# Performance work log

Hardware: AMD Instinct MI355X
Metric: run time of the kernel (lower is better)

The kernel has to match this reference:

```python
import jax, jax.numpy as jnp
import numpy as np

N = 10000
E = 640000


def setup_inputs() -> dict:
    key = jax.random.key(0)
    k = jax.random.split(key, 6)
    x = jax.random.normal(k[0], (N, 128), dtype=jnp.float32)
    edge_index = jax.random.randint(k[1], (2, E), 0, N, dtype=jnp.int64)
    # Linear weights stored as [in, out] (torch stores [out, in]; math is x @ W.T + b)
    w1 = jax.random.normal(k[2], (128, 128), dtype=jnp.float32) * 0.05
    b1 = jax.random.normal(k[3], (128,), dtype=jnp.float32) * 0.05
    w2 = jax.random.normal(k[4], (128, 128), dtype=jnp.float32) * 0.05
    b2 = jax.random.normal(k[5], (128,), dtype=jnp.float32) * 0.05
    return {"x": x, "edge_index": edge_index, "w1": w1, "b1": b1, "w2": w2, "b2": b2}


def gin_conv(x, src, dst, w, b, eps=0.0):
    # aggregate: out[i] = sum over edges (src->dst=i) of x[src]
    agg = jax.ops.segment_sum(x[src], dst, num_segments=N)  # [N, d]
    h = (1.0 + eps) * x + agg
    return h @ w + b


def reference(x, edge_index, w1, b1, w2, b2):
    src, dst = edge_index[0], edge_index[1]
    h = gin_conv(x, src, dst, w1, b1)
    h = jax.nn.relu(h)
    h = gin_conv(h, src, dst, w2, b2)
    return jax.nn.log_softmax(h, axis=1)
```

## Files before the change

### kernel.cpp

```cpp
#include <hip/hip_runtime.h>
#include <cstdint>

#define NNODES 10000
#define FDIM 128
#define MAXDEG 192
#define NPB 157
#define NBIN 64
#define BINCAP 16384

typedef _Float16 h2v  __attribute__((ext_vector_type(2)));
typedef _Float16 f16x8 __attribute__((ext_vector_type(8)));
typedef float    f32x4 __attribute__((ext_vector_type(4)));

__device__ __align__(16)  int            g_binoff[NBIN];
__device__ __align__(16)  unsigned       g_binbuf[NBIN * BINCAP];
__device__ __align__(16)  int            g_cnt[NNODES];
__device__ __align__(16)  unsigned short g_bkt[NNODES * MAXDEG];
__device__ __align__(256) unsigned g_xh [(NNODES + 1) * FDIM / 2];
__device__ __align__(256) unsigned g_h1h[(NNODES + 1) * FDIM / 2];
__device__ __align__(16)  unsigned g_wf[2 * 8192];

__device__ inline h2v as_h2(unsigned u) { return __builtin_bit_cast(h2v, u); }
__device__ inline unsigned as_u(h2v v) { return __builtin_bit_cast(unsigned, v); }
__device__ inline unsigned pack_f16x2(float a, float b) {
  h2v v; v[0] = (_Float16)a; v[1] = (_Float16)b;
  return as_u(v);
}
__device__ inline void vadd4(uint4& a, const uint4& b) {
  a.x = as_u(as_h2(a.x) + as_h2(b.x));
  a.y = as_u(as_h2(a.y) + as_h2(b.y));
  a.z = as_u(as_h2(a.z) + as_h2(b.z));
  a.w = as_u(as_h2(a.w) + as_h2(b.w));
}

__global__ __launch_bounds__(512) void prep1_kernel(
    const float* __restrict__ x, const int* __restrict__ ei,
    const float* __restrict__ w1, const float* __restrict__ w2,
    int E_, int PBLK) {
  const int bid = blockIdx.x, tid = threadIdx.x;
  if (bid < PBLK) {
    __shared__ int lcnt[NBIN], lbase[NBIN];
    if (tid < NBIN) lcnt[tid] = 0;
    __syncthreads();
    int dv[8], sv[8], rk[8], bn[8];
#pragma unroll
    for (int k = 0; k < 8; ++k) {
      int e = bid * 4096 + k * 512 + tid;
      dv[k] = (e < E_) ? ei[E_ + e] : -1;
      sv[k] = (e < E_) ? ei[e] : 0;
    }
#pragma unroll
    for (int k = 0; k < 8; ++k) {
      if (dv[k] >= 0) {
        bn[k] = (unsigned)dv[k] / NPB;
        rk[k] = atomicAdd(&lcnt[bn[k]], 1);
      }
    }
    __syncthreads();
    if (tid < NBIN && lcnt[tid] > 0)
      lbase[tid] = atomicAdd(&g_binoff[tid], lcnt[tid]);
    __syncthreads();
#pragma unroll
    for (int k = 0; k < 8; ++k) {
      if (dv[k] >= 0) {
        int pos = lbase[bn[k]] + rk[k];
        if (pos < BINCAP)
          g_binbuf[bn[k] * BINCAP + pos] =
              ((unsigned)(dv[k] - bn[k] * NPB) << 16) | (unsigned)sv[k];
      }
    }
  } else if (bid < PBLK + 625) {
    int i = (bid - PBLK) * 512 + tid;
    if (i < NNODES * 32) {
      float4 v = *(const float4*)(x + 4 * (size_t)i);
      uint2 o; o.x = pack_f16x2(v.x, v.y); o.y = pack_f16x2(v.z, v.w);
      *(uint2*)(g_xh + 2 * (size_t)i) = o;
    }
  } else {
    int idx = (bid - PBLK - 625) * 512 + tid;
    if (idx < 4096) {
      const float* w = (idx >= 2048) ? w2 : w1;
      int s = idx & 2047;
      int sl = s & 63, nk = s >> 6;
      int n = nk >> 2, kc = nk & 3;
      int kbase = kc * 32 + (sl >> 4) * 8;
      int f = n * 16 + (sl & 15);
      unsigned d0 = pack_f16x2(w[(size_t)(kbase + 0) * FDIM + f],
                               w[(size_t)(kbase + 1) * FDIM + f]);
      unsigned d1 = pack_f16x2(w[(size_t)(kbase + 2) * FDIM + f],
                               w[(size_t)(kbase + 3) * FDIM + f]);
      unsigned d2 = pack_f16x2(w[(size_t)(kbase + 4) * FDIM + f],
                               w[(size_t)(kbase + 5) * FDIM + f]);
      unsigned d3 = pack_f16x2(w[(size_t)(kbase + 6) * FDIM + f],
                               w[(size_t)(kbase + 7) * FDIM + f]);
      *(uint4*)(g_wf + (idx >> 11) * 8192 + 4 * s) = make_uint4(d0, d1, d2, d3);
    }
  }
}

__global__ __launch_bounds__(512) void prep2_kernel() {
  __shared__ int lcnt[NPB];
  __shared__ __align__(16) unsigned short lbkt[NPB * MAXDEG];

  const int bid = blockIdx.x, tid = threadIdx.x;
  const int lo = bid * NPB;
  const int nn = (NNODES - lo < NPB) ? (NNODES - lo) : NPB;
  for (int i = tid; i < NPB; i += 512) lcnt[i] = 0;
  __syncthreads();

  int cnt = g_binoff[bid];
  if (cnt > BINCAP) cnt = BINCAP;
  const unsigned* buf = g_binbuf + (size_t)bid * BINCAP;
  for (int i = tid; i < cnt; i += 512) {
    unsigned p = buf[i];
    int rel = (int)(p >> 16);
    if (rel < nn) {
      int q = atomicAdd(&lcnt[rel], 1);
      if (q < MAXDEG) lbkt[rel * MAXDEG + q] = (unsigned short)(p & 0xffffu);
    }
  }
  __syncthreads();

  for (int i = tid; i < nn; i += 512)
    g_cnt[lo + i] = (lcnt[i] > MAXDEG) ? MAXDEG : lcnt[i];
  const int nq = nn * (MAXDEG / 8);
  const uint4* srcq = (const uint4*)lbkt;
  uint4* dstq = (uint4*)(g_bkt + (size_t)lo * MAXDEG);
  for (int i = tid; i < nq; i += 512) dstq[i] = srcq[i];
  if (tid == 0) g_binoff[bid] = 0;
}

template <int MODE>
__global__ __launch_bounds__(512) void gin_layer_kernel(
    const float* __restrict__ bvec,
    float* __restrict__ out_g) {
  const unsigned* __restrict__ xh = (MODE == 0) ? g_xh : g_h1h;

  __shared__ __align__(16) unsigned al[16 * 68];
  __shared__ __align__(16) unsigned cfu[8 * 132];

  const int tid = threadIdx.x;
  const int wave = tid >> 6, lane = tid & 63;
  const int quad = lane >> 4, m16 = lane & 15;
  const int node0 = blockIdx.x * 8;
  const int myn = node0 + wave;

  uint4 bf[4];
  {
    const unsigned* wfp = g_wf + (MODE ? 8192 : 0);
#pragma unroll
    for (int kc = 0; kc < 4; ++kc)
      bf[kc] = *(const uint4*)(wfp + ((wave * 4 + kc) * 64 + lane) * 4);
  }
  const float bb = bvec[wave * 16 + m16];

  for (int i2 = tid; i2 < 8 * 68; i2 += 512) al[8 * 68 + i2] = 0;

  uint4 self4 = *(const uint4*)(xh + (size_t)myn * 64 + (m16 << 2));
  const int deg = g_cnt[myn];

  const unsigned short* nb16 = g_bkt + (size_t)myn * MAXDEG;
  int idxr[3];
#pragma unroll
  for (int r = 0; r < 3; ++r) {
    int g = r * 64 + lane;
    idxr[r] = (g < deg) ? (int)nb16[g] : NNODES;
  }

  h2v a0 = as_h2(0u), a1 = as_h2(0u), a2 = as_h2(0u), a3 = as_h2(0u);
  const int nbat = (deg + 31) >> 5;
  for (int bt = 0; bt < nbat; ++bt) {
    const int r = bt >> 1;
    const int src = (r == 0) ? idxr[0] : ((r == 1) ? idxr[1] : idxr[2]);
    const int base = (bt & 1) << 5;
    uint4 t[8];
#pragma unroll
    for (int k = 0; k < 8; ++k) {
      int e = __builtin_amdgcn_ds_bpermute((base + 4 * k + quad) << 2, src);
      t[k] = *(const uint4*)(xh + (unsigned)((e << 6) | (m16 << 2)));
    }
#pragma unroll
    for (int st2 = 1; st2 < 8; st2 <<= 1)
#pragma unroll
      for (int k = 0; k < 8; k += 2 * st2) vadd4(t[k], t[k + st2]);
    a0 += as_h2(t[0].x); a1 += as_h2(t[0].y);
    a2 += as_h2(t[0].z); a3 += as_h2(t[0].w);
  }

  int rr;
  rr = __shfl_xor((int)as_u(a0), 16, 64); a0 += as_h2((unsigned)rr);
  rr = __shfl_xor((int)as_u(a0), 32, 64); a0 += as_h2((unsigned)rr);
  rr = __shfl_xor((int)as_u(a1), 16, 64); a1 += as_h2((unsigned)rr);
  rr = __shfl_xor((int)as_u(a1), 32, 64); a1 += as_h2((unsigned)rr);
  rr = __shfl_xor((int)as_u(a2), 16, 64); a2 += as_h2((unsigned)rr);
  rr = __shfl_xor((int)as_u(a2), 32, 64); a2 += as_h2((unsigned)rr);
  rr = __shfl_xor((int)as_u(a3), 16, 64); a3 += as_h2((unsigned)rr);
  rr = __shfl_xor((int)as_u(a3), 32, 64); a3 += as_h2((unsigned)rr);
  a0 += as_h2(self4.x); a1 += as_h2(self4.y);
  a2 += as_h2(self4.z); a3 += as_h2(self4.w);
  if (quad == 0)
    *(uint4*)(al + wave * 68 + (m16 << 2)) =
        make_uint4(as_u(a0), as_u(a1), as_u(a2), as_u(a3));
  __syncthreads();

  uint4 af[4];
#pragma unroll
  for (int kc = 0; kc < 4; ++kc)
    af[kc] = *(const uint4*)(al + m16 * 68 + kc * 16 + quad * 4);

  const int n = wave;
  f32x4 acc = {0.f, 0.f, 0.f, 0.f};
#pragma unroll
  for (int kc = 0; kc < 4; ++kc)
    acc = __builtin_amdgcn_mfma_f32_16x16x32_f16(
            __builtin_bit_cast(f16x8, af[kc]),
            __builtin_bit_cast(f16x8, bf[kc]), acc, 0, 0, 0);

  if (MODE == 0) {
    _Float16* ch = (_Float16*)cfu;
    const int f = n * 16 + m16;
    if (quad < 2) {
#pragma unroll
      for (int reg = 0; reg < 4; ++reg)
        ch[(quad * 4 + reg) * 136 + f] = (_Float16)fmaxf(acc[reg] + bb, 0.f);
    }
    __syncthreads();
    if (tid < 256) {
      const int row = tid >> 5, c2 = (tid & 31) * 2;
      uint2 v = *(const uint2*)(cfu + row * 68 + c2);
      *(uint2*)(&g_h1h[(size_t)(node0 + row) * 64 + c2]) = v;
    }
  } else {
    float* cf = (float*)cfu;
    const int f = n * 16 + m16;
    if (quad < 2) {
#pragma unroll
      for (int reg = 0; reg < 4; ++reg)
        cf[(quad * 4 + reg) * 132 + f] = acc[reg] + bb;
    }
    __syncthreads();
    if (tid < 256) {
      const int row = tid >> 5, li = tid & 31;
      const float* base = cf + row * 132 + li * 4;
      float4 a4 = *(const float4*)(base);
      float mx = fmaxf(fmaxf(a4.x, a4.y), fmaxf(a4.z, a4.w));
#pragma unroll
      for (int off = 16; off >= 1; off >>= 1)
        mx = fmaxf(mx, __shfl_xor(mx, off, 64));
      float s = (__expf(a4.x - mx) + __expf(a4.y - mx))
              + (__expf(a4.z - mx) + __expf(a4.w - mx));
#pragma unroll
      for (int off = 16; off >= 1; off >>= 1)
        s += __shfl_xor(s, off, 64);
      const float ls = mx + __logf(s);
      float* orow = out_g + (size_t)(node0 + row) * FDIM + li * 4;
      *(float4*)(orow) = make_float4(a4.x - ls, a4.y - ls, a4.z - ls, a4.w - ls);
    }
  }
}

extern "C" void kernel_launch(void* const* d_in, const int* in_sizes, int n_in,
                              void* d_out, int out_size, void* d_ws, size_t ws_size,
                              hipStream_t stream) {
  const float* x  = (const float*)d_in[0];
  const int*   ei = (const int*)d_in[1];
  const float* w1 = (const float*)d_in[2];
  const float* b1 = (const float*)d_in[3];
  const float* w2 = (const float*)d_in[4];
  const float* b2 = (const float*)d_in[5];
  float* out = (float*)d_out;

  const int E_ = in_sizes[1] / 2;
  const int PBLK = (E_ + 4095) / 4096;

  prep1_kernel<<<PBLK + 625 + 8, 512, 0, stream>>>(x, ei, w1, w2, E_, PBLK);
  prep2_kernel<<<NBIN, 512, 0, stream>>>();

  gin_layer_kernel<0><<<1250, 512, 0, stream>>>(b1, nullptr);
  gin_layer_kernel<1><<<1250, 512, 0, stream>>>(b2, out);
}
```

Baseline: 108.1 us.

## Double bucket bins, move conversions to bucket pass, pre-fill sentinel neighbors

Halves nodes per bin (128 bins) so the bucket-fill stage runs on more blocks with less work each. The x and weight fp16 conversions move from the edge-binning kernel into the bucket kernel, letting the binning kernel run only edge blocks. Neighbor lists are pre-filled with a sentinel node index in shared memory, so the layer kernel loads indices without a per-lane degree check and issues those loads earlier. This adds a shared-memory fill per bin, and the smaller BINCAP raises the chance of overflow on skewed graphs.

```diff
diff --git a/kernel.cpp b/kernel.cpp
--- a/kernel.cpp
+++ b/kernel.cpp
@@ -4,9 +4,10 @@
 #define NNODES 10000
 #define FDIM 128
 #define MAXDEG 192
-#define NPB 157
-#define NBIN 64
-#define BINCAP 16384
+#define NPB 79
+#define NBIN 128
+#define BINCAP 6144
+#define SENT16 0x27102710u
 
 typedef _Float16 h2v  __attribute__((ext_vector_type(2)));
 typedef _Float16 f16x8 __attribute__((ext_vector_type(8)));
@@ -34,50 +35,87 @@
 }
 
 __global__ __launch_bounds__(512) void prep1_kernel(
-    const float* __restrict__ x, const int* __restrict__ ei,
-    const float* __restrict__ w1, const float* __restrict__ w2,
-    int E_, int PBLK) {
+    const int* __restrict__ ei, int E_) {
+  __shared__ int lcnt[NBIN], lbase[NBIN];
   const int bid = blockIdx.x, tid = threadIdx.x;
-  if (bid < PBLK) {
-    __shared__ int lcnt[NBIN], lbase[NBIN];
-    if (tid < NBIN) lcnt[tid] = 0;
-    __syncthreads();
-    int dv[8], sv[8], rk[8], bn[8];
-#pragma unroll
-    for (int k = 0; k < 8; ++k) {
-      int e = bid * 4096 + k * 512 + tid;
-      dv[k] = (e < E_) ? ei[E_ + e] : -1;
-      sv[k] = (e < E_) ? ei[e] : 0;
-    }
-#pragma unroll
-    for (int k = 0; k < 8; ++k) {
-      if (dv[k] >= 0) {
-        bn[k] = (unsigned)dv[k] / NPB;
-        rk[k] = atomicAdd(&lcnt[bn[k]], 1);
+  if (tid < NBIN) lcnt[tid] = 0;
+  __syncthreads();
+  int dv[8], sv[8], rk[8], bn[8];
+#pragma unroll
+  for (int k = 0; k < 8; ++k) {
+    int e = bid * 4096 + k * 512 + tid;
+    dv[k] = (e < E_) ? ei[E_ + e] : -1;
+    sv[k] = (e < E_) ? ei[e] : 0;
+  }
+#pragma unroll
+  for (int k = 0; k < 8; ++k) {
+    if (dv[k] >= 0) {
+      bn[k] = (unsigned)dv[k] / NPB;
+      rk[k] = atomicAdd(&lcnt[bn[k]], 1);
+    }
+  }
+  __syncthreads();
+  if (tid < NBIN && lcnt[tid] > 0)
+    lbase[tid] = atomicAdd(&g_binoff[tid], lcnt[tid]);
+  __syncthreads();
+#pragma unroll
+  for (int k = 0; k < 8; ++k) {
+    if (dv[k] >= 0) {
+      int pos = lbase[bn[k]] + rk[k];
+      if (pos < BINCAP)
+        g_binbuf[bn[k] * BINCAP + pos] =
+            ((unsigned)(dv[k] - bn[k] * NPB) << 16) | (unsigned)sv[k];
+    }
+  }
+}
+
+__global__ __launch_bounds__(512) void prep2_kernel(
+    const float* __restrict__ x,
+    const float* __restrict__ w1, const float* __restrict__ w2) {
+  const int bid = blockIdx.x, tid = threadIdx.x;
+  if (bid < NBIN) {
+    __shared__ int lcnt[NPB];
+    __shared__ __align__(16) unsigned short lbkt[NPB * MAXDEG];
+    const int lo = bid * NPB;
+    const int nnr = NNODES - lo;
+    const int nn = (nnr < 0) ? 0 : ((nnr < NPB) ? nnr : NPB);
+    for (int i = tid; i < NPB; i += 512) lcnt[i] = 0;
+    {
+      const uint4 sent = make_uint4(SENT16, SENT16, SENT16, SENT16);
+      uint4* lb4 = (uint4*)lbkt;
+      for (int i = tid; i < NPB * MAXDEG / 8; i += 512) lb4[i] = sent;
+    }
+    __syncthreads();
+
+    int cnt = g_binoff[bid];
+    if (cnt > BINCAP) cnt = BINCAP;
+    const unsigned* buf = g_binbuf + (size_t)bid * BINCAP;
+    for (int i = tid; i < cnt; i += 512) {
+      unsigned p = buf[i];
+      int rel = (int)(p >> 16);
+      if (rel < nn) {
+        int q = atomicAdd(&lcnt[rel], 1);
+        if (q < MAXDEG) lbkt[rel * MAXDEG + q] = (unsigned short)(p & 0xffffu);
       }
     }
     __syncthreads();
-    if (tid < NBIN && lcnt[tid] > 0)
-      lbase[tid] = atomicAdd(&g_binoff[tid], lcnt[tid]);
-    __syncthreads();
-#pragma unroll
-    for (int k = 0; k < 8; ++k) {
-      if (dv[k] >= 0) {
-        int pos = lbase[bn[k]] + rk[k];
-        if (pos < BINCAP)
-          g_binbuf[bn[k] * BINCAP + pos] =
-              ((unsigned)(dv[k] - bn[k] * NPB) << 16) | (unsigned)sv[k];
-      }
-    }
-  } else if (bid < PBLK + 625) {
-    int i = (bid - PBLK) * 512 + tid;
+
+    for (int i = tid; i < nn; i += 512)
+      g_cnt[lo + i] = (lcnt[i] > MAXDEG) ? MAXDEG : lcnt[i];
+    const int nq = nn * (MAXDEG / 8);
+    const uint4* srcq = (const uint4*)lbkt;
+    uint4* dstq = (uint4*)(g_bkt + (size_t)lo * MAXDEG);
+    for (int i = tid; i < nq; i += 512) dstq[i] = srcq[i];
+    if (tid == 0) g_binoff[bid] = 0;
+  } else if (bid < NBIN + 625) {
+    int i = (bid - NBIN) * 512 + tid;
     if (i < NNODES * 32) {
       float4 v = *(const float4*)(x + 4 * (size_t)i);
       uint2 o; o.x = pack_f16x2(v.x, v.y); o.y = pack_f16x2(v.z, v.w);
       *(uint2*)(g_xh + 2 * (size_t)i) = o;
     }
   } else {
-    int idx = (bid - PBLK - 625) * 512 + tid;
+    int idx = (bid - NBIN - 625) * 512 + tid;
     if (idx < 4096) {
       const float* w = (idx >= 2048) ? w2 : w1;
       int s = idx & 2047;
@@ -98,38 +136,6 @@
   }
 }
 
-__global__ __launch_bounds__(512) void prep2_kernel() {
-  __shared__ int lcnt[NPB];
-  __shared__ __align__(16) unsigned short lbkt[NPB * MAXDEG];
-
-  const int bid = blockIdx.x, tid = threadIdx.x;
-  const int lo = bid * NPB;
-  const int nn = (NNODES - lo < NPB) ? (NNODES - lo) : NPB;
-  for (int i = tid; i < NPB; i += 512) lcnt[i] = 0;
-  __syncthreads();
-
-  int cnt = g_binoff[bid];
-  if (cnt > BINCAP) cnt = BINCAP;
-  const unsigned* buf = g_binbuf + (size_t)bid * BINCAP;
-  for (int i = tid; i < cnt; i += 512) {
-    unsigned p = buf[i];
-    int rel = (int)(p >> 16);
-    if (rel < nn) {
-      int q = atomicAdd(&lcnt[rel], 1);
-      if (q < MAXDEG) lbkt[rel * MAXDEG + q] = (unsigned short)(p & 0xffffu);
-    }
-  }
-  __syncthreads();
-
-  for (int i = tid; i < nn; i += 512)
-    g_cnt[lo + i] = (lcnt[i] > MAXDEG) ? MAXDEG : lcnt[i];
-  const int nq = nn * (MAXDEG / 8);
-  const uint4* srcq = (const uint4*)lbkt;
-  uint4* dstq = (uint4*)(g_bkt + (size_t)lo * MAXDEG);
-  for (int i = tid; i < nq; i += 512) dstq[i] = srcq[i];
-  if (tid == 0) g_binoff[bid] = 0;
-}
-
 template <int MODE>
 __global__ __launch_bounds__(512) void gin_layer_kernel(
     const float* __restrict__ bvec,
@@ -145,6 +151,14 @@
   const int node0 = blockIdx.x * 8;
   const int myn = node0 + wave;
 
+  const unsigned short* nb16 = g_bkt + (size_t)myn * MAXDEG;
+  int idxr[3];
+#pragma unroll
+  for (int r = 0; r < 3; ++r)
+    idxr[r] = (int)nb16[r * 64 + lane];
+  const int deg = g_cnt[myn];
+  uint4 self4 = *(const uint4*)(xh + (size_t)myn * 64 + (m16 << 2));
+
   uint4 bf[4];
   {
     const unsigned* wfp = g_wf + (MODE ? 8192 : 0);
@@ -155,17 +169,6 @@
   const float bb = bvec[wave * 16 + m16];
 
   for (int i2 = tid; i2 < 8 * 68; i2 += 512) al[8 * 68 + i2] = 0;
-
-  uint4 self4 = *(const uint4*)(xh + (size_t)myn * 64 + (m16 << 2));
-  const int deg = g_cnt[myn];
-
-  const unsigned short* nb16 = g_bkt + (size_t)myn * MAXDEG;
-  int idxr[3];
-#pragma unroll
-  for (int r = 0; r < 3; ++r) {
-    int g = r * 64 + lane;
-    idxr[r] = (g < deg) ? (int)nb16[g] : NNODES;
-  }
 
   h2v a0 = as_h2(0u), a1 = as_h2(0u), a2 = as_h2(0u), a3 = as_h2(0u);
   const int nbat = (deg + 31) >> 5;
@@ -273,8 +276,8 @@
   const int E_ = in_sizes[1] / 2;
   const int PBLK = (E_ + 4095) / 4096;
 
-  prep1_kernel<<<PBLK + 625 + 8, 512, 0, stream>>>(x, ei, w1, w2, E_, PBLK);
-  prep2_kernel<<<NBIN, 512, 0, stream>>>();
+  prep1_kernel<<<PBLK, 512, 0, stream>>>(ei, E_);
+  prep2_kernel<<<NBIN + 625 + 8, 512, 0, stream>>>(x, w1, w2);
 
   gin_layer_kernel<0><<<1250, 512, 0, stream>>>(b1, nullptr);
   gin_layer_kernel<1><<<1250, 512, 0, stream>>>(b2, out);
```

New measurement: 105.4 us. -2.6%, faster.
